# Kernel tuning notes

Measured on AMD Instinct MI355X. Metric: run time of the kernel, lower is better.

Reference implementation:

```python
import jax, jax.numpy as jnp
import numpy as np

B, S = 4, 4096
DIM = 256
DF = 128   # dim_fourier = floor(256*0.5)
DS = 128   # dim_spline = 256 - 128
GF = 5     # fourier grid_size
GS = 5     # spline grid_size
K = 3      # spline order
P = 0.5
MIN_FREQ = 1e-6
LN_EPS = 1e-5


def _spline_grid():
    h = 2.0 / GS  # grid_range [-1, 1]
    g = np.arange(-K, GS + K + 1, dtype=np.float32) * h - 1.0
    return jnp.asarray(np.broadcast_to(g, (DS, g.shape[0])).copy())  # (DS, GS+2K+1)


def _base_freq():
    return jnp.asarray((1.0 / 10 ** np.linspace(0, 9, DF, dtype=np.float32)).reshape(DF, 1))


def b_splines(x, grid):
    # x: (N, DS); grid: (DS, GS+2K+1). Recursive de Boor B-spline basis.
    xe = x[:, :, None]
    bases = ((xe >= grid[:, :-1]) & (xe < grid[:, 1:])).astype(x.dtype)  # (N, DS, GS+2K)
    for k in range(1, K + 1):
        left = (xe - grid[:, : -(k + 1)]) / (grid[:, k:-1] - grid[:, : -(k + 1)])
        right = (grid[:, k + 1:] - xe) / (grid[:, k + 1:] - grid[:, 1:-k])
        bases = left * bases[:, :, :-1] + right * bases[:, :, 1:]
    return bases  # (N, DS, GS+K)


def setup_inputs() -> dict:
    key = jax.random.key(0)
    ks = jax.random.split(key, 8)
    timestamps = jax.random.uniform(ks[0], (B, S), dtype=jnp.float32)
    freq_theta = jnp.zeros((DF, 1), dtype=jnp.float32)
    bias_fourier = jnp.zeros((DF,), dtype=jnp.float32)
    fourier_weight = jax.random.normal(ks[1], (2, DF, DF, GF), dtype=jnp.float32) / (
        np.sqrt(DF) * np.sqrt(GF))
    w1_spline_w = jnp.asarray((1.0 / 10 ** np.linspace(0, 9, DS, dtype=np.float32)).reshape(DS, 1))
    w1_spline_b = jnp.zeros((DS,), dtype=jnp.float32)
    base_weight = jax.random.normal(ks[2], (DS, DS), dtype=jnp.float32) / np.sqrt(DS)
    spline_weight = jax.random.normal(ks[3], (DS, DS, GS + K), dtype=jnp.float32) / np.sqrt(DS * (GS + K))
    scale_weight = jnp.ones((DIM,), dtype=jnp.float32)
    ln_weight = jnp.ones((DIM,), dtype=jnp.float32)
    ln_bias = jnp.zeros((DIM,), dtype=jnp.float32)
    return {
        "timestamps": timestamps,
        "freq_theta": freq_theta,
        "bias_fourier": bias_fourier,
        "fourier_weight": fourier_weight,
        "w1_spline_w": w1_spline_w,
        "w1_spline_b": w1_spline_b,
        "base_weight": base_weight,
        "spline_weight": spline_weight,
        "scale_weight": scale_weight,
        "ln_weight": ln_weight,
        "ln_bias": ln_bias,
    }


def reference(timestamps, freq_theta, bias_fourier, fourier_weight,
              w1_spline_w, w1_spline_b, base_weight, spline_weight,
              scale_weight, ln_weight, ln_bias):
    grid = _spline_grid()
    base_freq = _base_freq()
    t = timestamps[..., None]  # (B, S, 1)

    # ---- Fourier branch ----
    freq_scale = jax.nn.softplus(freq_theta) + MIN_FREQ          # (DF, 1)
    freq_weight = base_freq * freq_scale                          # (DF, 1)
    proj_f = t * freq_weight[:, 0] + bias_fourier                 # (B, S, DF)
    xf = proj_f.reshape(-1, DF)                                   # (N, DF)
    kfreq = jnp.arange(1, GF + 1, dtype=xf.dtype)                 # (GF,)
    arg = xf[:, :, None] * kfreq                                  # (N, DF, GF)
    # Same math as torch's broadcast-then-sum, expressed as a contraction:
    # y[n,o] = sum_{d,g} cos(arg)[n,d,g] * Wc[o,d,g] + sin * Ws
    y_f = (jnp.einsum('ndg,odg->no', jnp.cos(arg), fourier_weight[0])
           + jnp.einsum('ndg,odg->no', jnp.sin(arg), fourier_weight[1])
           + fourier_weight[0].dtype.type(0) + jnp.zeros((DF,), xf.dtype))
    y_f = y_f  # bias of FourierSeries is zeros param; include explicitly below
    fourier_bias = jnp.zeros((DF,), xf.dtype)
    y_f = y_f + fourier_bias
    out_fourier = y_f.reshape(B, S, DF)

    # ---- Spline branch ----
    proj_s = t * w1_spline_w[:, 0] + w1_spline_b                  # (B, S, DS)
    xs = proj_s.reshape(-1, DS)                                   # (N, DS)
    base_out = jnp.tanh(xs) @ base_weight.T                       # (N, DS)
    bsp = b_splines(xs, grid).reshape(xs.shape[0], -1)            # (N, DS*(GS+K))
    spline_out = bsp @ spline_weight.reshape(DS, -1).T            # (N, DS)
    out_spline = (base_out + spline_out).reshape(B, S, DS)

    # ---- Combine (padded concat == concat of weighted halves) ----
    out = jnp.concatenate([out_fourier * P, out_spline * (1.0 - P)], axis=-1)  # (B, S, DIM)

    # LayerNorm then learnable scale
    mu = jnp.mean(out, axis=-1, keepdims=True)
    var = jnp.mean((out - mu) ** 2, axis=-1, keepdims=True)
    out = (out - mu) * jax.lax.rsqrt(var + LN_EPS) * ln_weight + ln_bias
    out = out * scale_weight
    return out
```

## Files before the change

kernel.cpp:

```cpp
#include <hip/hip_runtime.h>


typedef __attribute__((ext_vector_type(8))) _Float16 half8;
typedef __attribute__((ext_vector_type(2))) __fp16 fp16x2;
typedef __attribute__((ext_vector_type(16))) float f32x16;

#define KN5 -0.19999998807907104f
#define KN6  0.20000004768371582f
#define KN7  0.60000002384185791f

__device__ __forceinline__ unsigned pk(float a, float b) {
    fp16x2 h = __builtin_amdgcn_cvt_pkrtz(a, b);
    return __builtin_bit_cast(unsigned, h);
}

#define SPL9(x, o0,o1,o2,o3,o4,o5,o6,o7,o8) do {                          \
    float ax_ = fabsf(x);                                                  \
    float e_  = __expf(-2.f*ax_);                                          \
    float th_ = (1.f - e_) * __builtin_amdgcn_rcpf(1.f + e_);              \
    o0 = ((x) < 0.f) ? -th_ : th_;                                         \
    bool b1_ = ((x) >= KN6), b2_ = ((x) >= KN7);                           \
    float kn_ = b2_ ? KN7 : (b1_ ? KN6 : KN5);                             \
    float u_  = ((x) - kn_) * 2.5f;                                        \
    float um_ = 1.f - u_;                                                  \
    float u2_ = u_*u_, u3_ = u2_*u_, um2_ = um_*um_, um3_ = um2_*um_;      \
    float w0_ = (1.f/6.f)*um3_, w3_ = (1.f/6.f)*u3_;                       \
    float w1_ = 0.6666666666666667f - u2_  + 0.5f*u3_;                     \
    float w2_ = 0.6666666666666667f - um2_ + 0.5f*um3_;                    \
    o1 = 0.f; o2 = 0.f;                                                    \
    o3 = b1_ ? 0.f : w0_;                                                  \
    o4 = b2_ ? 0.f : (b1_ ? w0_ : w1_);                                    \
    o5 = b2_ ? w0_ : (b1_ ? w1_ : w2_);                                    \
    o6 = b2_ ? w1_ : (b1_ ? w2_ : w3_);                                    \
    o7 = b2_ ? w2_ : (b1_ ? w3_ : 0.f);                                    \
    o8 = b2_ ? w3_ : 0.f;                                                  \
} while (0)

__global__ __launch_bounds__(256) void prep_kernel(
    const float* __restrict__ FW,
    const float* __restrict__ BW,
    const float* __restrict__ SW,
    _Float16* __restrict__ WFP, _Float16* __restrict__ WSP)
{
    int tt = blockIdx.x * 256 + threadIdx.x;
    if (tt >= 327680) return;
    int e = tt & 7, l = (tt >> 3) & 63, frag = tt >> 9;
    int isS = frag >= 320;
    int f = isS ? frag - 320 : frag;
    int col = (f / 80) * 32 + (l & 31);
    int k = (f % 80) * 16 + (l >> 5) * 8 + e;
    int d = k / 10, j = k - d * 10;
    float val;
    if (!isS) {
        int p = (j >= 5), g = j - p * 5;
        val = FW[p * 81920 + col * 640 + d * 5 + g];
    } else {
        val = (j == 0) ? BW[col * 128 + d]
            : (j <= 8) ? SW[col * 1024 + d * 8 + (j - 1)] : 0.f;
    }
    (isS ? WSP : WFP)[(size_t)(f * 64 + l) * 8 + e] = (_Float16)val;
}

__global__ __launch_bounds__(512) void fused_kernel(
    const float* __restrict__ TS, const float* __restrict__ FTHETA,
    const float* __restrict__ BFOUR, const float* __restrict__ W1W,
    const float* __restrict__ W1B, const float* __restrict__ LNW,
    const float* __restrict__ LNB, const float* __restrict__ SCW,
    const _Float16* __restrict__ WFP, const _Float16* __restrict__ WSP,
    float* __restrict__ OUT)
{
    __shared__ __align__(16) char smem[32768];
    __shared__ float tsS[32], fwS[128], bfS[128], w1wS[128], w1bS[128];
    __shared__ float redS[32][8], redQ[32][8], muS[32], rsS[32];

    const int tid   = threadIdx.x;
    const int lane  = tid & 63;
    const int w     = tid >> 6;
    const int khalf = w >> 2, ct = w & 3;
    const int l31   = lane & 31, lh = lane >> 5;
    const int row0  = blockIdx.x * 32;

    _Float16* feat0 = (_Float16*)smem;
    _Float16* feat1 = (_Float16*)(smem + 10240);

    if (tid < 32) tsS[tid] = TS[row0 + tid];
    else if (tid >= 64 && tid < 192) {
        int d = tid - 64;
        float th = FTHETA[d];
        float sp = (th > 20.f) ? th : log1pf(__expf(th));
        float ex = (float)((double)d * (9.0 / 127.0));
        fwS[d] = (1.0f / powf(10.f, ex)) * (sp + 1e-6f);
        bfS[d] = BFOUR[d];
    } else if (tid >= 192 && tid < 320) {
        int d = tid - 192;
        w1wS[d] = W1W[d];
        w1bS[d] = W1B[d];
    }
    __syncthreads();

    const int dd   = tid & 15;
    const int frow = tid >> 4;
    const float tF = tsS[frow];
    const int bF = frow * 320 + dd * 20, swF = (frow & 7) << 4;
    const int abase = l31 * 320, aswz = (l31 & 7) << 4;

    f32x16 accF = {};
    f32x16 accS = {};

    auto computeFour = [&](int ch, _Float16* buf) {
        int d = ch * 16 + dd;
        float base = tF * fwS[d] + bfS[d];
        char* p = (char*)buf;
        float s1, c1;
        __sincosf(base, &s1, &c1);
        float tc = c1 + c1;
        float c2 = tc*c1 - 1.f, c3 = tc*c2 - c1, c4 = tc*c3 - c2, c5 = tc*c4 - c3;
        float s2 = tc*s1,       s3 = tc*s2 - s1, s4 = tc*s3 - s2, s5 = tc*s4 - s3;
        *(unsigned*)(p + ((bF +  0) ^ swF)) = pk(c1, c2);
        *(unsigned*)(p + ((bF +  4) ^ swF)) = pk(c3, c4);
        *(unsigned*)(p + ((bF +  8) ^ swF)) = pk(c5, s1);
        *(unsigned*)(p + ((bF + 12) ^ swF)) = pk(s2, s3);
        *(unsigned*)(p + ((bF + 16) ^ swF)) = pk(s4, s5);
    };

    auto computeSpl = [&](int ch, _Float16* buf) {
        int d = ch * 16 + dd;
        float x = tF * w1wS[d] + w1bS[d];
        char* p = (char*)buf;
        float t0,b0,b1,b2,b3,b4,b5,b6,b7;
        SPL9(x, t0,b0,b1,b2,b3,b4,b5,b6,b7);
        *(unsigned*)(p + ((bF +  0) ^ swF)) = pk(t0, b0);
        *(unsigned*)(p + ((bF +  4) ^ swF)) = pk(b1, b2);
        *(unsigned*)(p + ((bF +  8) ^ swF)) = pk(b3, b4);
        *(unsigned*)(p + ((bF + 12) ^ swF)) = pk(b5, b6);
        *(unsigned*)(p + ((bF + 16) ^ swF)) = pk(b7, 0.f);
    };

    auto mfmaF = [&](int ch, const _Float16* buf) {
        const char* p = (const char*)buf;
#pragma unroll
        for (int ks = 0; ks < 5; ++ks) {
            int ksg = khalf * 5 + ks;
            half8 b = *(const half8*)(WFP + (size_t)((ct*80 + ch*10 + ksg)*64 + lane) * 8);
            half8 a = *(const half8*)(p + ((abase + ksg*32 + lh*16) ^ aswz));
            accF = __builtin_amdgcn_mfma_f32_32x32x16_f16(a, b, accF, 0, 0, 0);
        }
    };

    auto mfmaS = [&](int ch, const _Float16* buf) {
        const char* p = (const char*)buf;
#pragma unroll
        for (int ks = 0; ks < 5; ++ks) {
            int ksg = khalf * 5 + ks;
            half8 b = *(const half8*)(WSP + (size_t)((ct*80 + ch*10 + ksg)*64 + lane) * 8);
            half8 a = *(const half8*)(p + ((abase + ksg*32 + lh*16) ^ aswz));
            accS = __builtin_amdgcn_mfma_f32_32x32x16_f16(a, b, accS, 0, 0, 0);
        }
    };

    computeFour(0, feat0);
    __syncthreads();
    for (int ph = 0; ph < 16; ++ph) {
        _Float16* nb = ((ph + 1) & 1) ? feat1 : feat0;
        const _Float16* cb = (ph & 1) ? feat1 : feat0;
        int nx = ph + 1;
        if (nx < 8)       computeFour(nx, nb);
        else if (nx < 16) computeSpl(nx - 8, nb);
        if (ph < 8) mfmaF(ph, cb);
        else        mfmaS(ph - 8, cb);
        __syncthreads();
    }

    float* part = (float*)smem;
#pragma unroll
    for (int g = 0; g < 16; ++g) {
        int r = (g & 3) + 8*(g >> 2) + 4*lh;
        if (khalf) part[(ct    )*1024 + r*32 + l31] = accF[g];
        else       part[(4 + ct)*1024 + r*32 + l31] = accS[g];
    }
    __syncthreads();
    f32x16 fin;
    const int colbase = khalf ? (128 + ct*32) : (ct*32);
#pragma unroll
    for (int g = 0; g < 16; ++g) {
        int r = (g & 3) + 8*(g >> 2) + 4*lh;
        float other = khalf ? part[(4 + ct)*1024 + r*32 + l31]
                            : part[(ct    )*1024 + r*32 + l31];
        fin[g] = 0.5f * ((khalf ? accS[g] : accF[g]) + other);
    }

#pragma unroll
    for (int g = 0; g < 16; ++g) {
        float s  = fin[g];
        float qq = fin[g] * fin[g];
#pragma unroll
        for (int m = 1; m < 32; m <<= 1) {
            s  += __shfl_xor(s, m);
            qq += __shfl_xor(qq, m);
        }
        if (l31 == 0) {
            int r = (g & 3) + 8*(g >> 2) + 4*lh;
            redS[r][w] = s;
            redQ[r][w] = qq;
        }
    }
    __syncthreads();
    if (tid < 32) {
        float s = 0.f, qq = 0.f;
#pragma unroll
        for (int wv = 0; wv < 8; ++wv) { s += redS[tid][wv]; qq += redQ[tid][wv]; }
        float mu = s * (1.0f / 256.0f);
        float var = qq * (1.0f / 256.0f) - mu * mu;
        muS[tid] = mu;
        rsS[tid] = rsqrtf(var + 1e-5f);
    }
    __syncthreads();
    {
        int c = colbase + l31;
        float gC = LNW[c] * SCW[c], hC = LNB[c] * SCW[c];
#pragma unroll
        for (int g = 0; g < 16; ++g) {
            int r = (g & 3) + 8*(g >> 2) + 4*lh;
            float mu = muS[r], rr = rsS[r];
            OUT[(size_t)(row0 + r) * 256 + c] = (fin[g] - mu) * rr * gC + hC;
        }
    }
}

extern "C" void kernel_launch(void* const* d_in, const int* in_sizes, int n_in,
                              void* d_out, int out_size, void* d_ws, size_t ws_size,
                              hipStream_t stream) {
    const float* TS     = (const float*)d_in[0];
    const float* FTHETA = (const float*)d_in[1];
    const float* BFOUR  = (const float*)d_in[2];
    const float* FW     = (const float*)d_in[3];
    const float* W1W    = (const float*)d_in[4];
    const float* W1B    = (const float*)d_in[5];
    const float* BW     = (const float*)d_in[6];
    const float* SW     = (const float*)d_in[7];
    const float* SCW    = (const float*)d_in[8];
    const float* LNW    = (const float*)d_in[9];
    const float* LNB    = (const float*)d_in[10];
    float* OUT = (float*)d_out;

    _Float16* WFP = (_Float16*)d_ws;
    _Float16* WSP = WFP + 163840;

    hipLaunchKernelGGL(prep_kernel, dim3(1280), dim3(256), 0, stream,
                       FW, BW, SW, WFP, WSP);
    hipLaunchKernelGGL(fused_kernel, dim3(512), dim3(512), 0, stream,
                       TS, FTHETA, BFOUR, W1W, W1B, LNW, LNB, SCW, WFP, WSP, OUT);
}
```

Before: 111.4 us.

## Merge Fourier and spline phases into one 8-step pipeline with prefetched weights

Each pipeline phase now computes both the Fourier and spline features for a chunk into a double-sized shared buffer, which halves the number of phases and barriers from 16 to 8. Weight fragments for both branches are loaded into registers before the feature computation, so the global loads overlap with the math. The two independent MFMA chains are interleaved to raise instruction-level parallelism. In exchange, shared memory per block goes from 32KB to 40KB and register pressure rises, and launch bounds now ask for 4 blocks per CU, which may force spills.

```diff
diff --git a/kernel.cpp b/kernel.cpp
--- a/kernel.cpp
+++ b/kernel.cpp
@@ -61,7 +61,7 @@
     (isS ? WSP : WFP)[(size_t)(f * 64 + l) * 8 + e] = (_Float16)val;
 }
 
-__global__ __launch_bounds__(512) void fused_kernel(
+__global__ __launch_bounds__(512, 4) void fused_kernel(
     const float* __restrict__ TS, const float* __restrict__ FTHETA,
     const float* __restrict__ BFOUR, const float* __restrict__ W1W,
     const float* __restrict__ W1B, const float* __restrict__ LNW,
@@ -69,7 +69,7 @@
     const _Float16* __restrict__ WFP, const _Float16* __restrict__ WSP,
     float* __restrict__ OUT)
 {
-    __shared__ __align__(16) char smem[32768];
+    __shared__ __align__(16) char smem[40960];
     __shared__ float tsS[32], fwS[128], bfS[128], w1wS[128], w1bS[128];
     __shared__ float redS[32][8], redQ[32][8], muS[32], rsS[32];
 
@@ -81,7 +81,7 @@
     const int row0  = blockIdx.x * 32;
 
     _Float16* feat0 = (_Float16*)smem;
-    _Float16* feat1 = (_Float16*)(smem + 10240);
+    _Float16* feat1 = (_Float16*)(smem + 20480);
 
     if (tid < 32) tsS[tid] = TS[row0 + tid];
     else if (tid >= 64 && tid < 192) {
@@ -101,73 +101,62 @@
     const int dd   = tid & 15;
     const int frow = tid >> 4;
     const float tF = tsS[frow];
-    const int bF = frow * 320 + dd * 20, swF = (frow & 7) << 4;
-    const int abase = l31 * 320, aswz = (l31 & 7) << 4;
+    const int bF = frow * 640 + dd * 20, swF = (frow & 7) << 4;
+    const int abase = l31 * 640, aswz = (l31 & 7) << 4;
 
     f32x16 accF = {};
     f32x16 accS = {};
 
-    auto computeFour = [&](int ch, _Float16* buf) {
+    auto computeFS = [&](int ch, _Float16* buf) {
         int d = ch * 16 + dd;
-        float base = tF * fwS[d] + bfS[d];
         char* p = (char*)buf;
-        float s1, c1;
-        __sincosf(base, &s1, &c1);
-        float tc = c1 + c1;
-        float c2 = tc*c1 - 1.f, c3 = tc*c2 - c1, c4 = tc*c3 - c2, c5 = tc*c4 - c3;
-        float s2 = tc*s1,       s3 = tc*s2 - s1, s4 = tc*s3 - s2, s5 = tc*s4 - s3;
-        *(unsigned*)(p + ((bF +  0) ^ swF)) = pk(c1, c2);
-        *(unsigned*)(p + ((bF +  4) ^ swF)) = pk(c3, c4);
-        *(unsigned*)(p + ((bF +  8) ^ swF)) = pk(c5, s1);
-        *(unsigned*)(p + ((bF + 12) ^ swF)) = pk(s2, s3);
-        *(unsigned*)(p + ((bF + 16) ^ swF)) = pk(s4, s5);
+        {
+            float base = tF * fwS[d] + bfS[d];
+            float s1, c1;
+            __sincosf(base, &s1, &c1);
+            float tc = c1 + c1;
+            float c2 = tc*c1 - 1.f, c3 = tc*c2 - c1, c4 = tc*c3 - c2, c5 = tc*c4 - c3;
+            float s2 = tc*s1,       s3 = tc*s2 - s1, s4 = tc*s3 - s2, s5 = tc*s4 - s3;
+            *(unsigned*)(p + ((bF +  0) ^ swF)) = pk(c1, c2);
+            *(unsigned*)(p + ((bF +  4) ^ swF)) = pk(c3, c4);
+            *(unsigned*)(p + ((bF +  8) ^ swF)) = pk(c5, s1);
+            *(unsigned*)(p + ((bF + 12) ^ swF)) = pk(s2, s3);
+            *(unsigned*)(p + ((bF + 16) ^ swF)) = pk(s4, s5);
+        }
+        {
+            float x = tF * w1wS[d] + w1bS[d];
+            float t0,b0,b1,b2,b3,b4,b5,b6,b7;
+            SPL9(x, t0,b0,b1,b2,b3,b4,b5,b6,b7);
+            int bS = bF + 320;
+            *(unsigned*)(p + ((bS +  0) ^ swF)) = pk(t0, b0);
+            *(unsigned*)(p + ((bS +  4) ^ swF)) = pk(b1, b2);
+            *(unsigned*)(p + ((bS +  8) ^ swF)) = pk(b3, b4);
+            *(unsigned*)(p + ((bS + 12) ^ swF)) = pk(b5, b6);
+            *(unsigned*)(p + ((bS + 16) ^ swF)) = pk(b7, 0.f);
+        }
     };
 
-    auto computeSpl = [&](int ch, _Float16* buf) {
-        int d = ch * 16 + dd;
-        float x = tF * w1wS[d] + w1bS[d];
-        char* p = (char*)buf;
-        float t0,b0,b1,b2,b3,b4,b5,b6,b7;
-        SPL9(x, t0,b0,b1,b2,b3,b4,b5,b6,b7);
-        *(unsigned*)(p + ((bF +  0) ^ swF)) = pk(t0, b0);
-        *(unsigned*)(p + ((bF +  4) ^ swF)) = pk(b1, b2);
-        *(unsigned*)(p + ((bF +  8) ^ swF)) = pk(b3, b4);
-        *(unsigned*)(p + ((bF + 12) ^ swF)) = pk(b5, b6);
-        *(unsigned*)(p + ((bF + 16) ^ swF)) = pk(b7, 0.f);
-    };
-
-    auto mfmaF = [&](int ch, const _Float16* buf) {
-        const char* p = (const char*)buf;
+    computeFS(0, feat0);
+    __syncthreads();
+    for (int ph = 0; ph < 8; ++ph) {
+        const char* cb = (const char*)((ph & 1) ? feat1 : feat0);
+        _Float16* nb = ((ph & 1) ? feat0 : feat1);
+        half8 BF[5], BS[5];
 #pragma unroll
         for (int ks = 0; ks < 5; ++ks) {
-            int ksg = khalf * 5 + ks;
-            half8 b = *(const half8*)(WFP + (size_t)((ct*80 + ch*10 + ksg)*64 + lane) * 8);
-            half8 a = *(const half8*)(p + ((abase + ksg*32 + lh*16) ^ aswz));
-            accF = __builtin_amdgcn_mfma_f32_32x32x16_f16(a, b, accF, 0, 0, 0);
-        }
-    };
-
-    auto mfmaS = [&](int ch, const _Float16* buf) {
-        const char* p = (const char*)buf;
+            int fi = ct*80 + ph*10 + khalf*5 + ks;
+            BF[ks] = *(const half8*)(WFP + (size_t)(fi*64 + lane) * 8);
+            BS[ks] = *(const half8*)(WSP + (size_t)(fi*64 + lane) * 8);
+        }
+        if (ph < 7) computeFS(ph + 1, nb);
 #pragma unroll
         for (int ks = 0; ks < 5; ++ks) {
-            int ksg = khalf * 5 + ks;
-            half8 b = *(const half8*)(WSP + (size_t)((ct*80 + ch*10 + ksg)*64 + lane) * 8);
-            half8 a = *(const half8*)(p + ((abase + ksg*32 + lh*16) ^ aswz));
-            accS = __builtin_amdgcn_mfma_f32_32x32x16_f16(a, b, accS, 0, 0, 0);
-        }
-    };
-
-    computeFour(0, feat0);
-    __syncthreads();
-    for (int ph = 0; ph < 16; ++ph) {
-        _Float16* nb = ((ph + 1) & 1) ? feat1 : feat0;
-        const _Float16* cb = (ph & 1) ? feat1 : feat0;
-        int nx = ph + 1;
-        if (nx < 8)       computeFour(nx, nb);
-        else if (nx < 16) computeSpl(nx - 8, nb);
-        if (ph < 8) mfmaF(ph, cb);
-        else        mfmaS(ph - 8, cb);
+            int ksg = khalf*5 + ks;
+            half8 aF = *(const half8*)(cb + ((abase +       ksg*32 + lh*16) ^ aswz));
+            half8 aS = *(const half8*)(cb + ((abase + 320 + ksg*32 + lh*16) ^ aswz));
+            accF = __builtin_amdgcn_mfma_f32_32x32x16_f16(aF, BF[ks], accF, 0, 0, 0);
+            accS = __builtin_amdgcn_mfma_f32_32x32x16_f16(aS, BS[ks], accS, 0, 0, 0);
+        }
         __syncthreads();
     }
 
```

After: 107.5 us. 1.04x faster.
